# Kernel tuning notes

Measured on AMD Instinct MI355X. Metric: run time of the kernel, lower is better.

## Reference

```python
import jax, jax.numpy as jnp
import numpy as np

B, S, DM, H = 4, 1024, 1024, 16
D = DM // H  # head size 64


def setup_inputs() -> dict:
    key = jax.random.key(0)
    ks = jax.random.split(key, 8)
    scale = 1.0 / np.sqrt(DM)
    return {
        "hidden_states": jax.random.normal(ks[0], (B, S, DM), dtype=jnp.float32),
        "attention_mask": jnp.zeros((B, 1, 1, S), dtype=jnp.float32),
        "link_mask": jax.random.uniform(ks[1], (B, 1, S, S), dtype=jnp.float32),
        "Wq": jax.random.normal(ks[2], (DM, DM), dtype=jnp.float32) * scale,
        "bq": jnp.zeros((DM,), dtype=jnp.float32),
        "Wk": jax.random.normal(ks[3], (DM, DM), dtype=jnp.float32) * scale,
        "bk": jnp.zeros((DM,), dtype=jnp.float32),
        "Wv": jax.random.normal(ks[4], (DM, DM), dtype=jnp.float32) * scale,
        "bv": jnp.zeros((DM,), dtype=jnp.float32),
    }


def _split_heads(x):
    # [B,S,DM] -> [B,H,S,D]
    return x.reshape(B, S, H, D).transpose(0, 2, 1, 3)


def reference(hidden_states, attention_mask, link_mask, Wq, bq, Wk, bk, Wv, bv):
    q = _split_heads(hidden_states @ Wq.T + bq)
    k = _split_heads(hidden_states @ Wk.T + bk)
    v = _split_heads(hidden_states @ Wv.T + bv)
    # [B,H,S,S]
    scores = jnp.einsum("bhqd,bhkd->bhqk", q, k) / jnp.float32(np.sqrt(D))
    scores = scores + attention_mask  # additive mask, broadcast [B,1,1,S]
    probs = jax.nn.softmax(scores, axis=-1)
    # post-softmax multiplicative link mask (un-normalizes rows)
    probs = probs * link_mask
    # dropout prob 0.0 (eval) -> identity
    ctx = jnp.einsum("bhqk,bhkd->bhqd", probs, v)
    ctx = ctx.transpose(0, 2, 1, 3).reshape(B, S, DM)
    return ctx
```

## Files before the change

kernel.cpp:

```cpp
#include <hip/hip_runtime.h>
#include <hip/hip_bf16.h>
#include <cstdint>

typedef __attribute__((ext_vector_type(8))) __bf16 bf16x8;
typedef __attribute__((ext_vector_type(4))) float f32x4;
typedef unsigned short u16;
typedef unsigned int u32;

struct alignas(8) U16x4 { u16 x, y, z, w; };
struct alignas(8) U32x2 { u32 x, y; };

__device__ __forceinline__ u16 f2b(float x) {
    u32 u = __builtin_bit_cast(u32, x);
    u += 0x7fffu + ((u >> 16) & 1u);
    return (u16)(u >> 16);
}
__device__ __forceinline__ u32 cvtpk(float lo, float hi) {
    u32 r;
    asm("v_cvt_pk_bf16_f32 %0, %1, %2" : "=v"(r) : "v"(lo), "v"(hi));
    return r;
}

__global__ __launch_bounds__(256) void cvt_kernel(
    const float* __restrict__ hs,
    const float* __restrict__ wq, const float* __restrict__ wk, const float* __restrict__ wv,
    u16* __restrict__ hsb, u16* __restrict__ wb)
{
    int i = blockIdx.x * 256 + threadIdx.x;
    const float4* src; u16* dst; int off;
    if (i < 1048576) { src = (const float4*)hs; dst = hsb; off = i; }
    else {
        int j = i - 1048576;
        int w = j >> 18;
        int o = j & 262143;
        src = (const float4*)(w == 0 ? wq : (w == 1 ? wk : wv));
        dst = wb + w * 1048576;
        off = o;
    }
    float4 v = src[off];
    U16x4 r; r.x = f2b(v.x); r.y = f2b(v.y); r.z = f2b(v.z); r.w = f2b(v.w);
    *(U16x4*)(dst + off * 4) = r;
}

__global__ __launch_bounds__(256, 3) void qkv_gemm(
    const u16* __restrict__ A, const u16* __restrict__ W,
    const float* __restrict__ bq, const float* __restrict__ bk, const float* __restrict__ bv,
    u16* __restrict__ Qo, u16* __restrict__ Ko, u16* __restrict__ Vt)
{
    __shared__ u16 As[2][128 * 32];
    __shared__ u16 Bs[2][128 * 32];
    const int tid = threadIdx.x;
    const int lane = tid & 63, wid = tid >> 6;
    const int wr = (wid >> 1) * 64, wc = (wid & 1) * 64;
    const int g = lane >> 4, c = lane & 15;

    int lin = blockIdx.y * 24 + blockIdx.x;
    int wg = (lin & 7) * 96 + (lin >> 3);
    const int bn = wg >> 5;
    const int bm = wg & 31;

    f32x4 acc[4][4] = {};

#define GSTAGE(bf, k0)                                                              \
    {                                                                               \
        _Pragma("unroll") for (int i = 0; i < 2; ++i) {                             \
            int chunk = i * 256 + tid;                                              \
            int row = chunk >> 2, col = (chunk & 3) * 8;                            \
            const u16* ga = A + (bm * 128 + row) * 1024 + (k0) + col;               \
            const u16* gb = W + (bn * 128 + row) * 1024 + (k0) + col;               \
            u16* la = &As[bf][0] + (i * 256 + wid * 64) * 8;                        \
            u16* lb = &Bs[bf][0] + (i * 256 + wid * 64) * 8;                        \
            __builtin_amdgcn_global_load_lds((const __attribute__((address_space(1))) u32*)ga, \
                                             (__attribute__((address_space(3))) u32*)la, 16, 0, 0); \
            __builtin_amdgcn_global_load_lds((const __attribute__((address_space(1))) u32*)gb, \
                                             (__attribute__((address_space(3))) u32*)lb, 16, 0, 0); \
        }                                                                           \
    }

    GSTAGE(0, 0);

    int cur = 0;
    for (int t = 0; t < 32; ++t) {
        __syncthreads();
        if (t < 31) GSTAGE(cur ^ 1, (t + 1) * 32);
        bf16x8 af[4], bf4[4];
        #pragma unroll
        for (int i = 0; i < 4; ++i)
            af[i] = *(const bf16x8*)(&As[cur][0] + (wr + i * 16 + c) * 32 + g * 8);
        #pragma unroll
        for (int j = 0; j < 4; ++j)
            bf4[j] = *(const bf16x8*)(&Bs[cur][0] + (wc + j * 16 + c) * 32 + g * 8);
        #pragma unroll
        for (int i = 0; i < 4; ++i)
            #pragma unroll
            for (int j = 0; j < 4; ++j)
                acc[i][j] = __builtin_amdgcn_mfma_f32_16x16x32_bf16(af[i], bf4[j], acc[i][j], 0, 0, 0);
        cur ^= 1;
    }
#undef GSTAGE

    const int region = bn >> 3;
    const float* bias = region == 0 ? bq : (region == 1 ? bk : bv);
    #pragma unroll
    for (int i = 0; i < 4; ++i) {
        int m0 = bm * 128 + wr + i * 16 + g * 4;
        int b = m0 >> 10, s0 = m0 & 1023;
        #pragma unroll
        for (int j = 0; j < 4; ++j) {
            int n = (bn & 7) * 128 + wc + j * 16 + c;
            float bb = bias[n];
            int h = n >> 6, d = n & 63;
            int bh = b * 16 + h;
            if (region == 2) {
                U16x4 pk;
                pk.x = f2b(acc[i][j][0] + bb);
                pk.y = f2b(acc[i][j][1] + bb);
                pk.z = f2b(acc[i][j][2] + bb);
                pk.w = f2b(acc[i][j][3] + bb);
                *(U16x4*)(Vt + (bh * 64 + d) * 1024 + s0) = pk;
            } else if (region == 1) {
                #pragma unroll
                for (int r = 0; r < 4; ++r)
                    Ko[(bh * 1024 + s0 + r) * 64 + d] = f2b(acc[i][j][r] + bb);
            } else {
                #pragma unroll
                for (int r = 0; r < 4; ++r)
                    Qo[(bh * 1024 + s0 + r) * 64 + d] = f2b((acc[i][j][r] + bb) * 0.125f);
            }
        }
    }
}

__global__ __launch_bounds__(256, 4) void attn_kernel(
    const u16* __restrict__ Q, const u16* __restrict__ K, const u16* __restrict__ Vt,
    const float* __restrict__ amask, const float* __restrict__ link,
    float* __restrict__ out)
{
    __shared__ u16 Ks[2][64 * 64];
    __shared__ u16 Vs[2][64 * 64];
    __shared__ u16 P[4][16 * 64];
    const int tid = threadIdx.x;
    const int lane = tid & 63, wid = tid >> 6;
    const int g = lane >> 4, c = lane & 15;
    const int c7 = c & 7;

    int hw = blockIdx.x;
    int logical = (hw & 7) * 128 + (hw >> 3);
    int b = logical >> 8;
    int qt = (logical >> 4) & 15;
    int h = logical & 15;
    int bh = b * 16 + h;
    const int qbase = qt * 64 + wid * 16;

    const u16* Qh = Q + bh * 65536;
    const u16* Kh = K + bh * 65536;
    const u16* Vh = Vt + bh * 65536;
    const float* mk = amask + b * 1024;
    const float* lkq = link + (size_t)b * 1048576 + (size_t)(qbase + c) * 1024;

    bf16x8 qfx0 = *(const bf16x8*)(Qh + (qbase + c) * 64 + g * 8);
    bf16x8 qfx1 = *(const bf16x8*)(Qh + (qbase + c) * 64 + 32 + g * 8);

    float lsum = 0.f;
    f32x4 ctx[4] = {};
    u16* const Pb = &P[wid][0];

#define ASTAGE(bf, kv)                                                              \
    {                                                                               \
        _Pragma("unroll") for (int i = 0; i < 2; ++i) {                             \
            int chunk = i * 256 + tid;                                              \
            int row = chunk >> 3;                                                   \
            int scir = (chunk & 7) ^ (row & 7);                                     \
            const u16* gk = Kh + ((kv) + row) * 64 + scir * 8;                      \
            const u16* gv = Vh + row * 1024 + (kv) + scir * 8;                      \
            u16* lk = &Ks[bf][0] + (i * 256 + wid * 64) * 8;                        \
            u16* lv = &Vs[bf][0] + (i * 256 + wid * 64) * 8;                        \
            __builtin_amdgcn_global_load_lds((const __attribute__((address_space(1))) u32*)gk, \
                                             (__attribute__((address_space(3))) u32*)lk, 16, 0, 0); \
            __builtin_amdgcn_global_load_lds((const __attribute__((address_space(1))) u32*)gv, \
                                             (__attribute__((address_space(3))) u32*)lv, 16, 0, 0); \
        }                                                                           \
    }

    ASTAGE(0, 0);

    int cur = 0;
    for (int t = 0; t < 16; ++t) {
        __syncthreads();
        if (t < 15) ASTAGE(cur ^ 1, (t + 1) * 64);
        const int kv = t * 64;
        const u16* Kb = &Ks[cur][0];
        const u16* Vb = &Vs[cur][0];

        f32x4 m4[4], lk4[4];
        #pragma unroll
        for (int kt = 0; kt < 4; ++kt) {
            m4[kt]  = *(const f32x4*)(mk  + kv + kt * 16 + g * 4);
            lk4[kt] = *(const f32x4*)(lkq + kv + kt * 16 + g * 4);
        }

        #pragma unroll
        for (int kt = 0; kt < 4; ++kt) {
            bf16x8 kf0 = *(const bf16x8*)(Kb + (kt * 16 + c) * 64 + ((g)     ^ c7) * 8);
            bf16x8 kf1 = *(const bf16x8*)(Kb + (kt * 16 + c) * 64 + ((4 + g) ^ c7) * 8);
            f32x4 sc = {};
            sc = __builtin_amdgcn_mfma_f32_16x16x32_bf16(kf0, qfx0, sc, 0, 0, 0);
            sc = __builtin_amdgcn_mfma_f32_16x16x32_bf16(kf1, qfx1, sc, 0, 0, 0);
            float e0 = __expf(sc[0] + m4[kt][0]);
            float e1 = __expf(sc[1] + m4[kt][1]);
            float e2 = __expf(sc[2] + m4[kt][2]);
            float e3 = __expf(sc[3] + m4[kt][3]);
            lsum += (e0 + e1) + (e2 + e3);
            U32x2 pw;
            pw.x = cvtpk(e0 * lk4[kt][0], e1 * lk4[kt][1]);
            pw.y = cvtpk(e2 * lk4[kt][2], e3 * lk4[kt][3]);
            *(U32x2*)(Pb + c * 64 + (((kt * 4 + g) ^ (c7 << 1)) * 4)) = pw;
        }
        __builtin_amdgcn_s_setprio(1);
        #pragma unroll
        for (int kk = 0; kk < 2; ++kk) {
            bf16x8 pf = *(const bf16x8*)(Pb + c * 64 + (((kk * 8 + g * 2) ^ (c7 << 1)) * 4));
            #pragma unroll
            for (int dt = 0; dt < 4; ++dt) {
                bf16x8 vf = *(const bf16x8*)(Vb + (dt * 16 + c) * 64 + ((kk * 4 + g) ^ c7) * 8);
                ctx[dt] = __builtin_amdgcn_mfma_f32_16x16x32_bf16(pf, vf, ctx[dt], 0, 0, 0);
            }
        }
        __builtin_amdgcn_s_setprio(0);
        cur ^= 1;
    }
#undef ASTAGE

    lsum += __shfl_xor(lsum, 16, 64);
    lsum += __shfl_xor(lsum, 32, 64);

    #pragma unroll
    for (int r = 0; r < 4; ++r) {
        float inv = 1.0f / __shfl(lsum, g * 4 + r, 16);
        int q = qbase + g * 4 + r;
        float* orow = out + (size_t)b * 1048576 + (size_t)q * 1024 + h * 64;
        #pragma unroll
        for (int dt = 0; dt < 4; ++dt)
            orow[dt * 16 + c] = ctx[dt][r] * inv;
    }
}

extern "C" void kernel_launch(void* const* d_in, const int* in_sizes, int n_in,
                              void* d_out, int out_size, void* d_ws, size_t ws_size,
                              hipStream_t stream)
{
    (void)in_sizes; (void)n_in; (void)out_size; (void)ws_size;
    const float* hs    = (const float*)d_in[0];
    const float* amask = (const float*)d_in[1];
    const float* link  = (const float*)d_in[2];
    const float* Wq    = (const float*)d_in[3];
    const float* bq    = (const float*)d_in[4];
    const float* Wk    = (const float*)d_in[5];
    const float* bk    = (const float*)d_in[6];
    const float* Wv    = (const float*)d_in[7];
    const float* bv    = (const float*)d_in[8];
    float* out = (float*)d_out;

    char* ws = (char*)d_ws;
    u16* hsb = (u16*)ws;
    u16* wb  = (u16*)(ws + (8u  << 20));
    u16* Qb  = (u16*)(ws + (14u << 20));
    u16* Kb  = (u16*)(ws + (22u << 20));
    u16* Vtb = (u16*)(ws + (30u << 20));

    cvt_kernel<<<7168, 256, 0, stream>>>(hs, Wq, Wk, Wv, hsb, wb);
    qkv_gemm<<<dim3(24, 32), 256, 0, stream>>>(hsb, wb, bq, bk, bv, Qb, Kb, Vtb);
    attn_kernel<<<1024, 256, 0, stream>>>(Qb, Kb, Vtb, amask, link, out);
}
```

Before: 97.42 us.

## Use 128-query attention blocks with 8 waves and exp2-based softmax

The attention kernel now runs 512 threads per block, covering 128 query rows instead of 64. Each K/V tile loaded into shared memory is therefore reused by twice as many waves, and the grid is halved. Separately, log2(e) is folded into the Q scaling and into a pre-scaled copy of the attention mask, so the softmax can call exp2f in place of __expf. The trade-offs are an extra tiny block in the conversion kernel, more shared memory per block, and occupancy limits set by the larger block.

```diff
diff --git a/kernel.cpp b/kernel.cpp
--- a/kernel.cpp
+++ b/kernel.cpp
@@ -21,11 +21,24 @@
     return r;
 }
 
+#define LOG2E 1.44269504088896f
+
 __global__ __launch_bounds__(256) void cvt_kernel(
     const float* __restrict__ hs,
     const float* __restrict__ wq, const float* __restrict__ wk, const float* __restrict__ wv,
-    u16* __restrict__ hsb, u16* __restrict__ wb)
-{
+    const float* __restrict__ amask,
+    u16* __restrict__ hsb, u16* __restrict__ wb, float* __restrict__ amask2)
+{
+    if (blockIdx.x == 7168) {
+        int t = threadIdx.x;
+        #pragma unroll
+        for (int j = 0; j < 4; ++j) {
+            float4 v = ((const float4*)amask)[t + j * 256];
+            v.x *= LOG2E; v.y *= LOG2E; v.z *= LOG2E; v.w *= LOG2E;
+            ((float4*)amask2)[t + j * 256] = v;
+        }
+        return;
+    }
     int i = blockIdx.x * 256 + threadIdx.x;
     const float4* src; u16* dst; int off;
     if (i < 1048576) { src = (const float4*)hs; dst = hsb; off = i; }
@@ -125,32 +138,32 @@
             } else {
                 #pragma unroll
                 for (int r = 0; r < 4; ++r)
-                    Qo[(bh * 1024 + s0 + r) * 64 + d] = f2b((acc[i][j][r] + bb) * 0.125f);
+                    Qo[(bh * 1024 + s0 + r) * 64 + d] = f2b((acc[i][j][r] + bb) * (0.125f * LOG2E));
             }
         }
     }
 }
 
-__global__ __launch_bounds__(256, 4) void attn_kernel(
+__global__ __launch_bounds__(512, 6) void attn_kernel(
     const u16* __restrict__ Q, const u16* __restrict__ K, const u16* __restrict__ Vt,
     const float* __restrict__ amask, const float* __restrict__ link,
     float* __restrict__ out)
 {
     __shared__ u16 Ks[2][64 * 64];
     __shared__ u16 Vs[2][64 * 64];
-    __shared__ u16 P[4][16 * 64];
+    __shared__ u16 P[8][16 * 64];
     const int tid = threadIdx.x;
     const int lane = tid & 63, wid = tid >> 6;
     const int g = lane >> 4, c = lane & 15;
     const int c7 = c & 7;
 
     int hw = blockIdx.x;
-    int logical = (hw & 7) * 128 + (hw >> 3);
-    int b = logical >> 8;
-    int qt = (logical >> 4) & 15;
+    int logical = (hw & 7) * 64 + (hw >> 3);
+    int b = logical >> 7;
+    int qt = (logical >> 4) & 7;
     int h = logical & 15;
     int bh = b * 16 + h;
-    const int qbase = qt * 64 + wid * 16;
+    const int qbase = qt * 128 + wid * 16;
 
     const u16* Qh = Q + bh * 65536;
     const u16* Kh = K + bh * 65536;
@@ -167,19 +180,17 @@
 
 #define ASTAGE(bf, kv)                                                              \
     {                                                                               \
-        _Pragma("unroll") for (int i = 0; i < 2; ++i) {                             \
-            int chunk = i * 256 + tid;                                              \
-            int row = chunk >> 3;                                                   \
-            int scir = (chunk & 7) ^ (row & 7);                                     \
-            const u16* gk = Kh + ((kv) + row) * 64 + scir * 8;                      \
-            const u16* gv = Vh + row * 1024 + (kv) + scir * 8;                      \
-            u16* lk = &Ks[bf][0] + (i * 256 + wid * 64) * 8;                        \
-            u16* lv = &Vs[bf][0] + (i * 256 + wid * 64) * 8;                        \
-            __builtin_amdgcn_global_load_lds((const __attribute__((address_space(1))) u32*)gk, \
-                                             (__attribute__((address_space(3))) u32*)lk, 16, 0, 0); \
-            __builtin_amdgcn_global_load_lds((const __attribute__((address_space(1))) u32*)gv, \
-                                             (__attribute__((address_space(3))) u32*)lv, 16, 0, 0); \
-        }                                                                           \
+        int chunk = tid;                                                            \
+        int row = chunk >> 3;                                                       \
+        int scir = (chunk & 7) ^ (row & 7);                                         \
+        const u16* gk = Kh + ((kv) + row) * 64 + scir * 8;                          \
+        const u16* gv = Vh + row * 1024 + (kv) + scir * 8;                          \
+        u16* lk = &Ks[bf][0] + (wid * 64) * 8;                                      \
+        u16* lv = &Vs[bf][0] + (wid * 64) * 8;                                      \
+        __builtin_amdgcn_global_load_lds((const __attribute__((address_space(1))) u32*)gk, \
+                                         (__attribute__((address_space(3))) u32*)lk, 16, 0, 0); \
+        __builtin_amdgcn_global_load_lds((const __attribute__((address_space(1))) u32*)gv, \
+                                         (__attribute__((address_space(3))) u32*)lv, 16, 0, 0); \
     }
 
     ASTAGE(0, 0);
@@ -206,10 +217,10 @@
             f32x4 sc = {};
             sc = __builtin_amdgcn_mfma_f32_16x16x32_bf16(kf0, qfx0, sc, 0, 0, 0);
             sc = __builtin_amdgcn_mfma_f32_16x16x32_bf16(kf1, qfx1, sc, 0, 0, 0);
-            float e0 = __expf(sc[0] + m4[kt][0]);
-            float e1 = __expf(sc[1] + m4[kt][1]);
-            float e2 = __expf(sc[2] + m4[kt][2]);
-            float e3 = __expf(sc[3] + m4[kt][3]);
+            float e0 = exp2f(sc[0] + m4[kt][0]);
+            float e1 = exp2f(sc[1] + m4[kt][1]);
+            float e2 = exp2f(sc[2] + m4[kt][2]);
+            float e3 = exp2f(sc[3] + m4[kt][3]);
             lsum += (e0 + e1) + (e2 + e3);
             U32x2 pw;
             pw.x = cvtpk(e0 * lk4[kt][0], e1 * lk4[kt][1]);
@@ -267,8 +278,9 @@
     u16* Qb  = (u16*)(ws + (14u << 20));
     u16* Kb  = (u16*)(ws + (22u << 20));
     u16* Vtb = (u16*)(ws + (30u << 20));
-
-    cvt_kernel<<<7168, 256, 0, stream>>>(hs, Wq, Wk, Wv, hsb, wb);
+    float* amask2 = (float*)(ws + (38u << 20));
+
+    cvt_kernel<<<7169, 256, 0, stream>>>(hs, Wq, Wk, Wv, amask, hsb, wb, amask2);
     qkv_gemm<<<dim3(24, 32), 256, 0, stream>>>(hsb, wb, bq, bk, bv, Qb, Kb, Vtb);
-    attn_kernel<<<1024, 256, 0, stream>>>(Qb, Kb, Vtb, amask, link, out);
-}
+    attn_kernel<<<512, 512, 0, stream>>>(Qb, Kb, Vtb, amask2, link, out);
+}
```

Result: slower. 119.6 us (+22.8%).
